# Optimization experiments

Measured on AMD Instinct MI355X. Metric: run time of the kernel, lower is better.

Reference implementation:

```python
import jax, jax.numpy as jnp
import numpy as np

D_MODEL = 768
NUM_HEADS = 12
HEAD_DIM = D_MODEL // NUM_HEADS
SEQ = 4096
BATCH = 1


def setup_inputs() -> dict:
    key = jax.random.key(0)
    ks = jax.random.split(key, 6)
    scale = 1.0 / np.sqrt(D_MODEL)
    x = jax.random.normal(ks[0], (BATCH, SEQ, D_MODEL), dtype=jnp.float32)
    mask = jnp.tril(jnp.ones((SEQ, SEQ), dtype=bool))[None, None]  # [1,1,S,S] causal
    Wq = jax.random.normal(ks[1], (D_MODEL, D_MODEL), dtype=jnp.float32) * scale
    Wk = jax.random.normal(ks[2], (D_MODEL, D_MODEL), dtype=jnp.float32) * scale
    Wv = jax.random.normal(ks[3], (D_MODEL, D_MODEL), dtype=jnp.float32) * scale
    Wo = jax.random.normal(ks[4], (D_MODEL, D_MODEL), dtype=jnp.float32) * scale
    bo = jax.random.normal(ks[5], (D_MODEL,), dtype=jnp.float32) * 0.01
    return {"x": x, "mask": mask, "Wq": Wq, "Wk": Wk, "Wv": Wv, "Wo": Wo, "bo": bo}


def _rope_tables(seq_len, head_dim, dtype):
    # inv_freq over even dims; emb = cat(freqs, freqs) but only the first half
    # participates in the well-defined rotation (x1/x2 have head_dim//2 channels)
    inv_freq = 1.0 / (10000.0 ** (jnp.arange(0, head_dim, 2, dtype=dtype) / head_dim))
    t = jnp.arange(seq_len, dtype=dtype)
    freqs = t[:, None] * inv_freq[None, :]  # [S, head_dim//2]
    return jnp.cos(freqs), jnp.sin(freqs)


def _apply_rotary(xh, cos, sin):
    # xh: [B,H,S,hd]; cos/sin: [S, hd//2]
    x1 = xh[..., ::2]
    x2 = xh[..., 1::2]
    # faithful to source: concatenated (not interleaved) rotated halves
    return jnp.concatenate([x1 * cos - x2 * sin, x1 * sin + x2 * cos], axis=-1)


def reference(x, mask, Wq, Wk, Wv, Wo, bo):
    B, S, D = x.shape
    H, hd = NUM_HEADS, HEAD_DIM
    def split_heads(y):
        return y.reshape(B, S, H, hd).transpose(0, 2, 1, 3)  # [B,H,S,hd]
    q = split_heads(x @ Wq.T)
    k = split_heads(x @ Wk.T)
    v = split_heads(x @ Wv.T)
    cos, sin = _rope_tables(S, hd, x.dtype)
    q = _apply_rotary(q, cos, sin)
    k = _apply_rotary(k, cos, sin)
    scores = jnp.einsum('bhqd,bhkd->bhqk', q, k) / jnp.sqrt(jnp.asarray(hd, x.dtype))
    scores = jnp.where(mask, scores, jnp.asarray(-1e9, x.dtype))
    attn = jax.nn.softmax(scores, axis=-1)  # dropout is identity in eval
    out = jnp.einsum('bhqk,bhkd->bhqd', attn, v)
    out = out.transpose(0, 2, 1, 3).reshape(B, S, D)
    return out @ Wo.T + bo
```

## Files before the change

### kernel.cpp

```cpp
#include <hip/hip_runtime.h>
#include <hip/hip_bf16.h>
#include <math.h>

#define SEQ 4096
#define DM  768
#define NH  12
#define HD  64
#define PER ((size_t)NH * SEQ * HD)
#define XN  ((size_t)SEQ * DM)
#define WN  ((size_t)DM * DM)

typedef __attribute__((ext_vector_type(8))) short bf16x8;
typedef __attribute__((ext_vector_type(4))) short s16x4;
typedef __attribute__((ext_vector_type(4))) float f32x4;

#define MFMA(a, b, c) __builtin_amdgcn_mfma_f32_16x16x32_bf16((a), (b), (c), 0, 0, 0)

#if __has_builtin(__builtin_amdgcn_exp2f)
#define EXP2(x) __builtin_amdgcn_exp2f(x)
#else
#define EXP2(x) exp2f(x)
#endif

#define SWZ(row, blk) (((row) << 6) + ((((blk) ^ ((row) & 7))) << 3))

__device__ __forceinline__ unsigned short f2b(float f) {
    unsigned int u = __float_as_uint(f);
    u += 0x7FFFu + ((u >> 16) & 1u);
    return (unsigned short)(u >> 16);
}

__global__ __launch_bounds__(256) void prep_kernel(
    const float* __restrict__ x,  const float* __restrict__ wq,
    const float* __restrict__ wk, const float* __restrict__ wv,
    const float* __restrict__ wo,
    unsigned short* __restrict__ dstbase, float2* __restrict__ rope)
{
    const float* srcs[5] = {x, wq, wk, wv, wo};
    const size_t n4s[5]  = {XN / 4, WN / 4, WN / 4, WN / 4, WN / 4};
    unsigned short* d = dstbase;
    for (int rg = 0; rg < 5; ++rg) {
        const float4* s4 = (const float4*)srcs[rg];
        s16x4* d4 = (s16x4*)d;
        for (size_t i = (size_t)blockIdx.x * 256 + threadIdx.x; i < n4s[rg];
             i += (size_t)gridDim.x * 256) {
            const float4 v = s4[i];
            s16x4 p;
            p.x = (short)f2b(v.x); p.y = (short)f2b(v.y);
            p.z = (short)f2b(v.z); p.w = (short)f2b(v.w);
            d4[i] = p;
        }
        d += n4s[rg] * 4;
    }
    for (int g = blockIdx.x * 256 + threadIdx.x; g < 131072; g += gridDim.x * 256) {
        const int row = g >> 5, fi = g & 31;
        const float invf = expf(-(float)fi * 0.28782313662425576f);
        float sn, cs;
        sincosf((float)row * invf, &sn, &cs);
        rope[row * 32 + fi] = make_float2(cs, sn);
    }
}

__global__ __launch_bounds__(256) void qkv_mfma(
    const float* __restrict__ x,  const unsigned short* __restrict__ xb,
    const float* __restrict__ Wq, const float* __restrict__ Wk, const float* __restrict__ Wv,
    const unsigned short* __restrict__ Wqb, const unsigned short* __restrict__ Wkb,
    const unsigned short* __restrict__ Wvb,
    const float2* __restrict__ rope,
    unsigned short* __restrict__ Qo, unsigned short* __restrict__ Ko,
    unsigned short* __restrict__ Vo, int fast)
{
    __shared__ __align__(16) unsigned short Xs[2][4096];
    __shared__ __align__(16) unsigned short Ws[2][3][4096];
    __shared__ unsigned short VL[64 * 66];

    const int t    = threadIdx.x;
    const int w    = t >> 6;
    const int lane = t & 63;
    const int quad = lane >> 4;
    const int l16  = lane & 15;

    const int gid = blockIdx.y * 64 + blockIdx.x;
    const int Wl  = (gid & 7) * 96 + (gid >> 3);
    const int h   = Wl % 12;
    const int s0  = (Wl / 12) * 64;
    const int n0  = h * 64;

    const unsigned short* Wbs[3] = {Wqb, Wkb, Wvb};
    const float*          Wfs[3] = {Wq, Wk, Wv};

    const int rowb = 32 * (w >> 1);
    const int colb = 32 * (w & 1);

    f32x4 acc[3][2][2];
    #pragma unroll
    for (int rg = 0; rg < 3; ++rg)
        #pragma unroll
        for (int mi = 0; mi < 2; ++mi)
            #pragma unroll
            for (int ni = 0; ni < 2; ++ni) acc[rg][mi][ni] = (f32x4){0,0,0,0};

    const int prow = t >> 3, pblk = t & 7;

    bf16x8 xr0, xr1, wr0[3], wr1[3];
    if (fast) {
        xr0 = *(const bf16x8*)&xb[(size_t)(s0 + prow) * DM + pblk * 8];
        xr1 = *(const bf16x8*)&xb[(size_t)(s0 + prow + 32) * DM + pblk * 8];
        #pragma unroll
        for (int rg = 0; rg < 3; ++rg) {
            wr0[rg] = *(const bf16x8*)&Wbs[rg][(size_t)(n0 + prow) * DM + pblk * 8];
            wr1[rg] = *(const bf16x8*)&Wbs[rg][(size_t)(n0 + prow + 32) * DM + pblk * 8];
        }
        *(bf16x8*)&Xs[0][SWZ(prow, pblk)]      = xr0;
        *(bf16x8*)&Xs[0][SWZ(prow + 32, pblk)] = xr1;
        #pragma unroll
        for (int rg = 0; rg < 3; ++rg) {
            *(bf16x8*)&Ws[0][rg][SWZ(prow, pblk)]      = wr0[rg];
            *(bf16x8*)&Ws[0][rg][SWZ(prow + 32, pblk)] = wr1[rg];
        }
    } else {
        for (int e = t; e < 1024; e += 256) {
            const int row = e >> 4, c4 = e & 15;
            const int off = SWZ(row, c4 >> 1) + (c4 & 1) * 4;
            const float4 xv = *(const float4*)&x[(size_t)(s0 + row) * DM + c4 * 4];
            s16x4 px; px.x = (short)f2b(xv.x); px.y = (short)f2b(xv.y);
            px.z = (short)f2b(xv.z); px.w = (short)f2b(xv.w);
            *(s16x4*)&Xs[0][off] = px;
            #pragma unroll
            for (int rg = 0; rg < 3; ++rg) {
                const float4 wv = *(const float4*)&Wfs[rg][(size_t)(n0 + row) * DM + c4 * 4];
                s16x4 pw; pw.x = (short)f2b(wv.x); pw.y = (short)f2b(wv.y);
                pw.z = (short)f2b(wv.z); pw.w = (short)f2b(wv.w);
                *(s16x4*)&Ws[0][rg][off] = pw;
            }
        }
    }
    __syncthreads();

    for (int kt = 0; kt < 12; ++kt) {
        const unsigned short* Xb = Xs[kt & 1];
        if (fast && kt < 11) {
            const int k0 = (kt + 1) * 64;
            xr0 = *(const bf16x8*)&xb[(size_t)(s0 + prow) * DM + k0 + pblk * 8];
            xr1 = *(const bf16x8*)&xb[(size_t)(s0 + prow + 32) * DM + k0 + pblk * 8];
            #pragma unroll
            for (int rg = 0; rg < 3; ++rg) {
                wr0[rg] = *(const bf16x8*)&Wbs[rg][(size_t)(n0 + prow) * DM + k0 + pblk * 8];
                wr1[rg] = *(const bf16x8*)&Wbs[rg][(size_t)(n0 + prow + 32) * DM + k0 + pblk * 8];
            }
        }
        bf16x8 a[2][2];
        #pragma unroll
        for (int mi = 0; mi < 2; ++mi)
            #pragma unroll
            for (int hh = 0; hh < 2; ++hh)
                a[mi][hh] = *(const bf16x8*)&Xb[SWZ(rowb + 16 * mi + l16, 4 * hh + quad)];
        #pragma unroll
        for (int rg = 0; rg < 3; ++rg) {
            const unsigned short* Wbt = Ws[kt & 1][rg];
            #pragma unroll
            for (int ni = 0; ni < 2; ++ni) {
                const bf16x8 b0 = *(const bf16x8*)&Wbt[SWZ(colb + 16 * ni + l16, quad)];
                const bf16x8 b1 = *(const bf16x8*)&Wbt[SWZ(colb + 16 * ni + l16, 4 + quad)];
                #pragma unroll
                for (int mi = 0; mi < 2; ++mi) {
                    acc[rg][mi][ni] = MFMA(a[mi][0], b0, acc[rg][mi][ni]);
                    acc[rg][mi][ni] = MFMA(a[mi][1], b1, acc[rg][mi][ni]);
                }
            }
        }
        if (kt < 11) {
            const int nb = (kt + 1) & 1;
            if (fast) {
                *(bf16x8*)&Xs[nb][SWZ(prow, pblk)]      = xr0;
                *(bf16x8*)&Xs[nb][SWZ(prow + 32, pblk)] = xr1;
                #pragma unroll
                for (int rg = 0; rg < 3; ++rg) {
                    *(bf16x8*)&Ws[nb][rg][SWZ(prow, pblk)]      = wr0[rg];
                    *(bf16x8*)&Ws[nb][rg][SWZ(prow + 32, pblk)] = wr1[rg];
                }
            } else {
                const int k0 = (kt + 1) * 64;
                for (int e = t; e < 1024; e += 256) {
                    const int row = e >> 4, c4 = e & 15;
                    const int off = SWZ(row, c4 >> 1) + (c4 & 1) * 4;
                    const float4 xv = *(const float4*)&x[(size_t)(s0 + row) * DM + k0 + c4 * 4];
                    s16x4 px; px.x = (short)f2b(xv.x); px.y = (short)f2b(xv.y);
                    px.z = (short)f2b(xv.z); px.w = (short)f2b(xv.w);
                    *(s16x4*)&Xs[nb][off] = px;
                    #pragma unroll
                    for (int rg = 0; rg < 3; ++rg) {
                        const float4 wv = *(const float4*)&Wfs[rg][(size_t)(n0 + row) * DM + k0 + c4 * 4];
                        s16x4 pw; pw.x = (short)f2b(wv.x); pw.y = (short)f2b(wv.y);
                        pw.z = (short)f2b(wv.z); pw.w = (short)f2b(wv.w);
                        *(s16x4*)&Ws[nb][rg][off] = pw;
                    }
                }
            }
        }
        __syncthreads();
    }

    const size_t headoff = (size_t)h * SEQ * HD;
    #pragma unroll
    for (int rg = 0; rg < 2; ++rg) {
        unsigned short* dst = (rg == 0) ? Qo : Ko;
        const float qsc = (rg == 0) ? 0.18033688011112042f : 1.0f;
        #pragma unroll
        for (int mi = 0; mi < 2; ++mi)
            #pragma unroll
            for (int ni = 0; ni < 2; ++ni)
                #pragma unroll
                for (int r = 0; r < 4; ++r) {
                    const int srow = s0 + rowb + 16 * mi + quad * 4 + r;
                    const int d  = colb + 16 * ni + l16;
                    const int fi = d >> 1;
                    const float own = acc[rg][mi][ni][r] * qsc;
                    const float oth = __shfl_xor(own, 1);
                    float cs, sn;
                    if (fast) {
                        const float2 t2 = rope[srow * 32 + fi];
                        cs = t2.x; sn = t2.y;
                    } else {
                        const float invf = expf(-(float)fi * 0.28782313662425576f);
                        sincosf((float)srow * invf, &sn, &cs);
                    }
                    const float val = (d & 1) ? (oth * sn + own * cs)
                                              : (own * cs - oth * sn);
                    dst[headoff + (size_t)srow * HD + ((d & 1) ? 32 : 0) + fi] = f2b(val);
                }
    }
    #pragma unroll
    for (int mi = 0; mi < 2; ++mi)
        #pragma unroll
        for (int ni = 0; ni < 2; ++ni)
            #pragma unroll
            for (int r = 0; r < 4; ++r)
                VL[(colb + 16 * ni + l16) * 66 + rowb + 16 * mi + quad * 4 + r] =
                    f2b(acc[2][mi][ni][r]);
    __syncthreads();
    for (int e = t; e < 2048; e += 256) {
        const int d = e >> 5, sp = e & 31;
        const unsigned int v = (unsigned int)VL[d * 66 + 2 * sp] |
                               ((unsigned int)VL[d * 66 + 2 * sp + 1] << 16);
        *(unsigned int*)&Vo[headoff + (size_t)d * SEQ + s0 + 2 * sp] = v;
    }
}

__global__ __launch_bounds__(256, 2) void attn_mfma(
    const unsigned short* __restrict__ Q,
    const unsigned short* __restrict__ K,
    const unsigned short* __restrict__ V,
    unsigned short* __restrict__ O,
    float* __restrict__ Part)
{
    __shared__ __align__(16) unsigned char SM[39936];
    unsigned short* Ps  = (unsigned short*)SM;
    unsigned short* Qst = (unsigned short*)(SM + 20480);
    float* ACC  = (float*)SM;
    float* ACC2 = (float*)(SM + 20480);
    float* Lx   = (float*)(SM + 38912);

    int h, xx;
    if (gridDim.x == 96) {
        const int gid = blockIdx.y * 96 + blockIdx.x;
        const int Wl  = (gid & 7) * 144 + (gid >> 3);
        h  = Wl / 96;
        xx = Wl - h * 96;
    } else {
        const int gid = blockIdx.y * 64 + blockIdx.x;
        const int Wl  = (gid & 7) * 96 + (gid >> 3);
        h  = Wl >> 6;
        xx = Wl & 63;
    }

    int i, kstart, nch, domask, partial, pslice;
    if (gridDim.x == 96) {
        if (xx < 64) {
            i = 63 - xx; kstart = 0;
            const int full = ((i * 64 + 63) >> 7) + 1;
            nch = full < 16 ? full : 16;
            domask  = (i <= 31);
            partial = (i >= 32); pslice = 0;
        } else {
            i = 127 - xx; kstart = 2048;
            nch = ((i * 64 + 63 - 2048) >> 7) + 1;
            domask = 1; partial = 1; pslice = 1;
        }
    } else {
        i = 63 - xx; kstart = 0;
        nch = ((i * 64 + 63) >> 7) + 1;
        domask = 1; partial = 0; pslice = 0;
    }
    const int q0 = i * 64;

    const int t    = threadIdx.x;
    const int w    = t >> 6;
    const int lane = t & 63;
    const int quad = lane >> 4;
    const int l16  = lane & 15;
    const size_t headoff = (size_t)h * SEQ * HD;
    const unsigned short* Kg = K + headoff;
    const unsigned short* Vg = V + headoff;

    for (int e = t; e < 512; e += 256) {
        const int row = e >> 3, bp = e & 7, blk = bp ^ (row & 7);
        *(bf16x8*)&Qst[row * 64 + bp * 8] =
            *(const bf16x8*)&Q[headoff + (size_t)(q0 + row) * HD + blk * 8];
    }
    __syncthreads();
    bf16x8 aQ[4][2];
    #pragma unroll
    for (int qt = 0; qt < 4; ++qt)
        #pragma unroll
        for (int hh = 0; hh < 2; ++hh)
            aQ[qt][hh] = *(const bf16x8*)&Qst[SWZ(16 * qt + l16, 4 * hh + quad)];

    bf16x8 kf00, kf01, kf10, kf11;
    {
        const size_t kr = (size_t)(kstart + 32 * w + l16) * HD + quad * 8;
        kf00 = *(const bf16x8*)&Kg[kr];
        kf01 = *(const bf16x8*)&Kg[kr + 32];
        kf10 = *(const bf16x8*)&Kg[kr + 16 * HD];
        kf11 = *(const bf16x8*)&Kg[kr + 16 * HD + 32];
    }

    bf16x8 ones;
    #pragma unroll
    for (int ii = 0; ii < 8; ++ii) ones[ii] = (short)0x3F80;

    f32x4 oT[4][4];
    #pragma unroll
    for (int dt = 0; dt < 4; ++dt)
        #pragma unroll
        for (int qt = 0; qt < 4; ++qt) oT[dt][qt] = (f32x4){0,0,0,0};
    f32x4 lT[4] = {{0,0,0,0},{0,0,0,0},{0,0,0,0},{0,0,0,0}};

    unsigned short* usp = Ps + w * 2560;

    for (int c = 0; c < nch; ++c) {
        const int k0 = kstart + c * 128;
        const int last = (c == nch - 1);

        const size_t vr = (size_t)l16 * SEQ + k0 + 32 * w + quad * 8;
        const bf16x8 vf0 = *(const bf16x8*)&Vg[vr];
        const bf16x8 vf1 = *(const bf16x8*)&Vg[vr + 16 * SEQ];
        const bf16x8 vf2 = *(const bf16x8*)&Vg[vr + 32 * SEQ];
        const bf16x8 vf3 = *(const bf16x8*)&Vg[vr + 48 * SEQ];

        #pragma unroll
        for (int qt = 0; qt < 4; ++qt) {
            f32x4 s0 = (f32x4){0,0,0,0}, s1 = (f32x4){0,0,0,0};
            s0 = MFMA(aQ[qt][0], kf00, s0);
            s0 = MFMA(aQ[qt][1], kf01, s0);
            s1 = MFMA(aQ[qt][0], kf10, s1);
            s1 = MFMA(aQ[qt][1], kf11, s1);
            if (domask && last) {
                const int key0 = k0 + 32 * w + l16;
                #pragma unroll
                for (int r = 0; r < 4; ++r) {
                    const int qrow = q0 + 16 * qt + 4 * quad + r;
                    if (key0 > qrow)      s0[r] = -1e30f;
                    if (key0 + 16 > qrow) s1[r] = -1e30f;
                }
            }
            #pragma unroll
            for (int r = 0; r < 4; ++r) {
                const int row = (16 * qt + 4 * quad + r) * 40;
                usp[row + l16]      = f2b(EXP2(s0[r]));
                usp[row + 16 + l16] = f2b(EXP2(s1[r]));
            }
        }

        if (c + 1 < nch) {
            const size_t kr = (size_t)(k0 + 128 + 32 * w + l16) * HD + quad * 8;
            kf00 = *(const bf16x8*)&Kg[kr];
            kf01 = *(const bf16x8*)&Kg[kr + 32];
            kf10 = *(const bf16x8*)&Kg[kr + 16 * HD];
            kf11 = *(const bf16x8*)&Kg[kr + 16 * HD + 32];
        }

        asm volatile("s_waitcnt lgkmcnt(0)" ::: "memory");

        __builtin_amdgcn_s_setprio(1);
        #pragma unroll
        for (int qt = 0; qt < 4; ++qt) {
            const bf16x8 bP = *(const bf16x8*)&usp[(16 * qt + l16) * 40 + quad * 8];
            lT[qt] = MFMA(ones, bP, lT[qt]);
            oT[0][qt] = MFMA(vf0, bP, oT[0][qt]);
            oT[1][qt] = MFMA(vf1, bP, oT[1][qt]);
            oT[2][qt] = MFMA(vf2, bP, oT[2][qt]);
            oT[3][qt] = MFMA(vf3, bP, oT[3][qt]);
        }
        __builtin_amdgcn_s_setprio(0);
    }

    __syncthreads();
    if (w != 0 && quad == 0) {
        #pragma unroll
        for (int qt = 0; qt < 4; ++qt)
            Lx[w * 64 + 16 * qt + l16] = lT[qt][0];
    }
    if (w == 1) {
        #pragma unroll
        for (int dt = 0; dt < 4; ++dt)
            #pragma unroll
            for (int qt = 0; qt < 4; ++qt)
                *(f32x4*)&ACC[(16 * qt + l16) * 72 + 16 * dt + 4 * quad] = oT[dt][qt];
    }
    __syncthreads();
    if (w == 0) {
        #pragma unroll
        for (int dt = 0; dt < 4; ++dt)
            #pragma unroll
            for (int qt = 0; qt < 4; ++qt)
                oT[dt][qt] += *(const f32x4*)&ACC[(16 * qt + l16) * 72 + 16 * dt + 4 * quad];
    }
    if (w == 2) {
        #pragma unroll
        for (int dt = 0; dt < 4; ++dt)
            #pragma unroll
            for (int qt = 0; qt < 4; ++qt)
                *(f32x4*)&ACC2[(16 * qt + l16) * 72 + 16 * dt + 4 * quad] = oT[dt][qt];
    }
    __syncthreads();
    if (w == 0) {
        #pragma unroll
        for (int dt = 0; dt < 4; ++dt)
            #pragma unroll
            for (int qt = 0; qt < 4; ++qt)
                oT[dt][qt] += *(const f32x4*)&ACC2[(16 * qt + l16) * 72 + 16 * dt + 4 * quad];
    }
    if (w == 3) {
        #pragma unroll
        for (int dt = 0; dt < 4; ++dt)
            #pragma unroll
            for (int qt = 0; qt < 4; ++qt)
                *(f32x4*)&ACC[(16 * qt + l16) * 72 + 16 * dt + 4 * quad] = oT[dt][qt];
    }
    __syncthreads();
    if (w == 0) {
        float ls[4];
        #pragma unroll
        for (int qt = 0; qt < 4; ++qt) {
            #pragma unroll
            for (int dt = 0; dt < 4; ++dt)
                oT[dt][qt] += *(const f32x4*)&ACC[(16 * qt + l16) * 72 + 16 * dt + 4 * quad];
            ls[qt] = lT[qt][0] + Lx[64 + 16 * qt + l16] +
                     Lx[128 + 16 * qt + l16] + Lx[192 + 16 * qt + l16];
        }
        if (!partial) {
            #pragma unroll
            for (int qt = 0; qt < 4; ++qt) {
                const float inv = 1.0f / ls[qt];
                const size_t rowoff = (size_t)(q0 + 16 * qt + l16) * DM + h * HD;
                #pragma unroll
                for (int dt = 0; dt < 4; ++dt) {
                    ushort4 u;
                    u.x = f2b(oT[dt][qt][0] * inv);
                    u.y = f2b(oT[dt][qt][1] * inv);
                    u.z = f2b(oT[dt][qt][2] * inv);
                    u.w = f2b(oT[dt][qt][3] * inv);
                    *(ushort4*)&O[rowoff + 16 * dt + 4 * quad] = u;
                }
            }
        } else {
            float* P = Part + (size_t)(((i - 32) * 12 + h) * 2 + pslice) * 4160;
            #pragma unroll
            for (int dt = 0; dt < 4; ++dt)
                #pragma unroll
                for (int qt = 0; qt < 4; ++qt)
                    *(f32x4*)&P[(16 * qt + l16) * 64 + 16 * dt + 4 * quad] = oT[dt][qt];
            if (quad == 0) {
                #pragma unroll
                for (int qt = 0; qt < 4; ++qt)
                    P[4096 + 16 * qt + l16] = ls[qt];
            }
        }
    }
}

__global__ __launch_bounds__(256) void reduce_attn(
    const float* __restrict__ Part, unsigned short* __restrict__ O)
{
    const int b  = blockIdx.x;
    const int i  = 32 + b / 12, h = b % 12;
    const int q0 = i * 64;
    const float* P0 = Part + (size_t)(b * 2 + 0) * 4160;
    const float* P1 = Part + (size_t)(b * 2 + 1) * 4160;
    __shared__ float linv[64];
    const int t = threadIdx.x;
    if (t < 64) linv[t] = 1.0f / (P0[4096 + t] + P1[4096 + t]);
    __syncthreads();
    for (int idx = t; idx < 4096; idx += 256) {
        const int q = idx >> 6, d = idx & 63;
        const float v = (P0[q * 64 + d] + P1[q * 64 + d]) * linv[q];
        O[(size_t)(q0 + q) * DM + h * HD + d] = f2b(v);
    }
}

__global__ __launch_bounds__(256) void proj_mfma(
    const unsigned short* __restrict__ A,
    const float* __restrict__ Wo, const unsigned short* __restrict__ Wob,
    const float* __restrict__ bo,
    float* __restrict__ out, int fast)
{
    __shared__ __align__(16) unsigned short Xs[2][4096];
    __shared__ __align__(16) unsigned short Ws[2][4096];

    const int t    = threadIdx.x;
    const int w    = t >> 6;
    const int lane = t & 63;
    const int quad = lane >> 4;
    const int l16  = lane & 15;

    const int gid = blockIdx.y * 64 + blockIdx.x;
    const int Wl  = (gid & 7) * 96 + (gid >> 3);
    const int s0  = (Wl / 12) * 64;
    const int n0  = (Wl % 12) * 64;

    const int prow = t >> 3, pblk = t & 7;

    f32x4 acc[4] = {{0,0,0,0},{0,0,0,0},{0,0,0,0},{0,0,0,0}};

    bf16x8 ar0, ar1, wr0, wr1;
    ar0 = *(const bf16x8*)&A[(size_t)(s0 + prow) * DM + pblk * 8];
    ar1 = *(const bf16x8*)&A[(size_t)(s0 + prow + 32) * DM + pblk * 8];
    *(bf16x8*)&Xs[0][SWZ(prow, pblk)]      = ar0;
    *(bf16x8*)&Xs[0][SWZ(prow + 32, pblk)] = ar1;
    if (fast) {
        wr0 = *(const bf16x8*)&Wob[(size_t)(n0 + prow) * DM + pblk * 8];
        wr1 = *(const bf16x8*)&Wob[(size_t)(n0 + prow + 32) * DM + pblk * 8];
        *(bf16x8*)&Ws[0][SWZ(prow, pblk)]      = wr0;
        *(bf16x8*)&Ws[0][SWZ(prow + 32, pblk)] = wr1;
    } else {
        for (int e = t; e < 1024; e += 256) {
            const int row = e >> 4, c4 = e & 15;
            const float4 wv = *(const float4*)&Wo[(size_t)(n0 + row) * DM + c4 * 4];
            s16x4 pw; pw.x = (short)f2b(wv.x); pw.y = (short)f2b(wv.y);
            pw.z = (short)f2b(wv.z); pw.w = (short)f2b(wv.w);
            *(s16x4*)&Ws[0][SWZ(row, c4 >> 1) + (c4 & 1) * 4] = pw;
        }
    }
    __syncthreads();

    for (int kt = 0; kt < 12; ++kt) {
        const unsigned short* Xb  = Xs[kt & 1];
        const unsigned short* Wbt = Ws[kt & 1];
        if (kt < 11) {
            const int k0 = (kt + 1) * 64;
            ar0 = *(const bf16x8*)&A[(size_t)(s0 + prow) * DM + k0 + pblk * 8];
            ar1 = *(const bf16x8*)&A[(size_t)(s0 + prow + 32) * DM + k0 + pblk * 8];
            if (fast) {
                wr0 = *(const bf16x8*)&Wob[(size_t)(n0 + prow) * DM + k0 + pblk * 8];
                wr1 = *(const bf16x8*)&Wob[(size_t)(n0 + prow + 32) * DM + k0 + pblk * 8];
            }
        }
        const bf16x8 a0 = *(const bf16x8*)&Xb[SWZ(16 * w + l16, quad)];
        const bf16x8 a1 = *(const bf16x8*)&Xb[SWZ(16 * w + l16, 4 + quad)];
        #pragma unroll
        for (int nt = 0; nt < 4; ++nt) {
            const bf16x8 b0 = *(const bf16x8*)&Wbt[SWZ(16 * nt + l16, quad)];
            const bf16x8 b1 = *(const bf16x8*)&Wbt[SWZ(16 * nt + l16, 4 + quad)];
            acc[nt] = MFMA(a0, b0, acc[nt]);
            acc[nt] = MFMA(a1, b1, acc[nt]);
        }
        if (kt < 11) {
            const int nb = (kt + 1) & 1;
            *(bf16x8*)&Xs[nb][SWZ(prow, pblk)]      = ar0;
            *(bf16x8*)&Xs[nb][SWZ(prow + 32, pblk)] = ar1;
            if (fast) {
                *(bf16x8*)&Ws[nb][SWZ(prow, pblk)]      = wr0;
                *(bf16x8*)&Ws[nb][SWZ(prow + 32, pblk)] = wr1;
            } else {
                const int k0 = (kt + 1) * 64;
                for (int e = t; e < 1024; e += 256) {
                    const int row = e >> 4, c4 = e & 15;
                    const float4 wv = *(const float4*)&Wo[(size_t)(n0 + row) * DM + k0 + c4 * 4];
                    s16x4 pw; pw.x = (short)f2b(wv.x); pw.y = (short)f2b(wv.y);
                    pw.z = (short)f2b(wv.z); pw.w = (short)f2b(wv.w);
                    *(s16x4*)&Ws[nb][SWZ(row, c4 >> 1) + (c4 & 1) * 4] = pw;
                }
            }
        }
        __syncthreads();
    }

    #pragma unroll
    for (int nt = 0; nt < 4; ++nt)
        #pragma unroll
        for (int r = 0; r < 4; ++r) {
            const int srow = s0 + 16 * w + quad * 4 + r;
            const int n    = n0 + nt * 16 + l16;
            out[(size_t)srow * DM + n] = acc[nt][r] + bo[n];
        }
}

extern "C" void kernel_launch(void* const* d_in, const int* in_sizes, int n_in,
                              void* d_out, int out_size, void* d_ws, size_t ws_size,
                              hipStream_t stream) {
    const float* x  = (const float*)d_in[0];
    const float* Wq = (const float*)d_in[2];
    const float* Wk = (const float*)d_in[3];
    const float* Wv = (const float*)d_in[4];
    const float* Wo = (const float*)d_in[5];
    const float* bo = (const float*)d_in[6];
    float* out = (float*)d_out;

    unsigned short* U  = (unsigned short*)d_ws;
    unsigned short* Qw = U;
    unsigned short* Kw = U + PER;
    unsigned short* Vw = U + 2 * PER;
    unsigned short* Ow = U + 3 * PER;
    unsigned short* xb  = U + 4 * PER;
    unsigned short* Wqb = xb + XN;
    unsigned short* Wkb = Wqb + WN;
    unsigned short* Wvb = Wkb + WN;
    unsigned short* Wob = Wvb + WN;
    float2* rope = (float2*)(Wob + WN);
    float*  part = (float*)(rope + 4096 * 32);
    const size_t need  = (char*)part - (char*)d_ws;
    const size_t need2 = need + (size_t)384 * 2 * 4160 * 4;
    const int fast  = (ws_size >= need)  ? 1 : 0;
    const int split = (ws_size >= need2) ? 1 : 0;

    if (fast)
        prep_kernel<<<1024, 256, 0, stream>>>(x, Wq, Wk, Wv, Wo, xb, rope);
    qkv_mfma<<<dim3(64, 12), 256, 0, stream>>>(
        x, xb, Wq, Wk, Wv, Wqb, Wkb, Wvb, rope, Qw, Kw, Vw, fast);
    if (split) {
        attn_mfma<<<dim3(96, NH), 256, 0, stream>>>(Qw, Kw, Vw, Ow, part);
        reduce_attn<<<dim3(384), 256, 0, stream>>>(part, Ow);
    } else {
        attn_mfma<<<dim3(64, 12), 256, 0, stream>>>(Qw, Kw, Vw, Ow, part);
    }
    proj_mfma<<<dim3(SEQ / 64, DM / 64), 256, 0, stream>>>(Ow, Wo, Wob, bo, out, fast);
}
```

Measured before the change: 233.5 us.

## Software-pipeline QK scores one chunk ahead in attention inner loop

Restructures the attention key-chunk loop so the QK^T MFMAs for the next chunk are issued while the current chunk's exp/store to LDS runs, using ping-pong score register arrays. K is now prefetched two chunks ahead and V one chunk ahead, after the PV MFMAs. The aim is to hide global-load and MFMA latency behind the softmax exp work. The cost is higher register pressure (16 extra f32x4) and a manually unrolled loop body, which may lower occupancy.

After: 235.7 us. About the same (+0.9%).

```diff
diff --git a/kernel.cpp b/kernel.cpp
--- a/kernel.cpp
+++ b/kernel.cpp
@@ -324,6 +324,31 @@
         kf10 = *(const bf16x8*)&Kg[kr + 16 * HD];
         kf11 = *(const bf16x8*)&Kg[kr + 16 * HD + 32];
     }
+    f32x4 sA[8], sB[8];
+    #pragma unroll
+    for (int qt = 0; qt < 4; ++qt) {
+        f32x4 s0 = (f32x4){0,0,0,0}, s1 = (f32x4){0,0,0,0};
+        s0 = MFMA(aQ[qt][0], kf00, s0);
+        s0 = MFMA(aQ[qt][1], kf01, s0);
+        s1 = MFMA(aQ[qt][0], kf10, s1);
+        s1 = MFMA(aQ[qt][1], kf11, s1);
+        sA[2 * qt] = s0; sA[2 * qt + 1] = s1;
+    }
+    bf16x8 vf0, vf1, vf2, vf3;
+    {
+        const size_t vr = (size_t)l16 * SEQ + kstart + 32 * w + quad * 8;
+        vf0 = *(const bf16x8*)&Vg[vr];
+        vf1 = *(const bf16x8*)&Vg[vr + 16 * SEQ];
+        vf2 = *(const bf16x8*)&Vg[vr + 32 * SEQ];
+        vf3 = *(const bf16x8*)&Vg[vr + 48 * SEQ];
+    }
+    if (nch > 1) {
+        const size_t kr = (size_t)(kstart + 128 + 32 * w + l16) * HD + quad * 8;
+        kf00 = *(const bf16x8*)&Kg[kr];
+        kf01 = *(const bf16x8*)&Kg[kr + 32];
+        kf10 = *(const bf16x8*)&Kg[kr + 16 * HD];
+        kf11 = *(const bf16x8*)&Kg[kr + 16 * HD + 32];
+    }
 
     bf16x8 ones;
     #pragma unroll
@@ -338,62 +363,70 @@
 
     unsigned short* usp = Ps + w * 2560;
 
-    for (int c = 0; c < nch; ++c) {
-        const int k0 = kstart + c * 128;
-        const int last = (c == nch - 1);
-
-        const size_t vr = (size_t)l16 * SEQ + k0 + 32 * w + quad * 8;
-        const bf16x8 vf0 = *(const bf16x8*)&Vg[vr];
-        const bf16x8 vf1 = *(const bf16x8*)&Vg[vr + 16 * SEQ];
-        const bf16x8 vf2 = *(const bf16x8*)&Vg[vr + 32 * SEQ];
-        const bf16x8 vf3 = *(const bf16x8*)&Vg[vr + 48 * SEQ];
-
-        #pragma unroll
-        for (int qt = 0; qt < 4; ++qt) {
-            f32x4 s0 = (f32x4){0,0,0,0}, s1 = (f32x4){0,0,0,0};
-            s0 = MFMA(aQ[qt][0], kf00, s0);
-            s0 = MFMA(aQ[qt][1], kf01, s0);
-            s1 = MFMA(aQ[qt][0], kf10, s1);
-            s1 = MFMA(aQ[qt][1], kf11, s1);
-            if (domask && last) {
-                const int key0 = k0 + 32 * w + l16;
-                #pragma unroll
-                for (int r = 0; r < 4; ++r) {
-                    const int qrow = q0 + 16 * qt + 4 * quad + r;
-                    if (key0 > qrow)      s0[r] = -1e30f;
-                    if (key0 + 16 > qrow) s1[r] = -1e30f;
-                }
-            }
-            #pragma unroll
-            for (int r = 0; r < 4; ++r) {
-                const int row = (16 * qt + 4 * quad + r) * 40;
-                usp[row + l16]      = f2b(EXP2(s0[r]));
-                usp[row + 16 + l16] = f2b(EXP2(s1[r]));
-            }
-        }
-
-        if (c + 1 < nch) {
-            const size_t kr = (size_t)(k0 + 128 + 32 * w + l16) * HD + quad * 8;
-            kf00 = *(const bf16x8*)&Kg[kr];
-            kf01 = *(const bf16x8*)&Kg[kr + 32];
-            kf10 = *(const bf16x8*)&Kg[kr + 16 * HD];
-            kf11 = *(const bf16x8*)&Kg[kr + 16 * HD + 32];
-        }
-
-        asm volatile("s_waitcnt lgkmcnt(0)" ::: "memory");
-
-        __builtin_amdgcn_s_setprio(1);
-        #pragma unroll
-        for (int qt = 0; qt < 4; ++qt) {
-            const bf16x8 bP = *(const bf16x8*)&usp[(16 * qt + l16) * 40 + quad * 8];
-            lT[qt] = MFMA(ones, bP, lT[qt]);
-            oT[0][qt] = MFMA(vf0, bP, oT[0][qt]);
-            oT[1][qt] = MFMA(vf1, bP, oT[1][qt]);
-            oT[2][qt] = MFMA(vf2, bP, oT[2][qt]);
-            oT[3][qt] = MFMA(vf3, bP, oT[3][qt]);
-        }
-        __builtin_amdgcn_s_setprio(0);
-    }
+#define STEP(cur, nxt, cc) do {                                               \
+    const int k0_   = kstart + (cc) * 128;                                    \
+    const int last_ = ((cc) == nch - 1);                                      \
+    const int hasN_ = ((cc) + 1 < nch);                                       \
+    _Pragma("unroll")                                                         \
+    for (int qt = 0; qt < 4; ++qt) {                                          \
+        f32x4 s0 = cur[2 * qt], s1 = cur[2 * qt + 1];                         \
+        if (domask && last_) {                                                \
+            const int key0 = k0_ + 32 * w + l16;                              \
+            _Pragma("unroll")                                                 \
+            for (int r = 0; r < 4; ++r) {                                     \
+                const int qrow = q0 + 16 * qt + 4 * quad + r;                 \
+                if (key0 > qrow)      s0[r] = -1e30f;                         \
+                if (key0 + 16 > qrow) s1[r] = -1e30f;                         \
+            }                                                                 \
+        }                                                                     \
+        _Pragma("unroll")                                                     \
+        for (int r = 0; r < 4; ++r) {                                         \
+            const int row_ = (16 * qt + 4 * quad + r) * 40;                   \
+            usp[row_ + l16]      = f2b(EXP2(s0[r]));                          \
+            usp[row_ + 16 + l16] = f2b(EXP2(s1[r]));                          \
+        }                                                                     \
+        if (hasN_) {                                                          \
+            f32x4 n0 = (f32x4){0,0,0,0}, n1 = (f32x4){0,0,0,0};               \
+            n0 = MFMA(aQ[qt][0], kf00, n0);                                   \
+            n0 = MFMA(aQ[qt][1], kf01, n0);                                   \
+            n1 = MFMA(aQ[qt][0], kf10, n1);                                   \
+            n1 = MFMA(aQ[qt][1], kf11, n1);                                   \
+            nxt[2 * qt] = n0; nxt[2 * qt + 1] = n1;                           \
+        }                                                                     \
+    }                                                                         \
+    if ((cc) + 2 < nch) {                                                     \
+        const size_t kr_ = (size_t)(k0_ + 256 + 32 * w + l16) * HD + quad * 8;\
+        kf00 = *(const bf16x8*)&Kg[kr_];                                      \
+        kf01 = *(const bf16x8*)&Kg[kr_ + 32];                                 \
+        kf10 = *(const bf16x8*)&Kg[kr_ + 16 * HD];                            \
+        kf11 = *(const bf16x8*)&Kg[kr_ + 16 * HD + 32];                       \
+    }                                                                         \
+    asm volatile("s_waitcnt lgkmcnt(0)" ::: "memory");                        \
+    __builtin_amdgcn_s_setprio(1);                                            \
+    _Pragma("unroll")                                                         \
+    for (int qt = 0; qt < 4; ++qt) {                                          \
+        const bf16x8 bP = *(const bf16x8*)&usp[(16 * qt + l16) * 40 + quad * 8];\
+        lT[qt] = MFMA(ones, bP, lT[qt]);                                      \
+        oT[0][qt] = MFMA(vf0, bP, oT[0][qt]);                                 \
+        oT[1][qt] = MFMA(vf1, bP, oT[1][qt]);                                 \
+        oT[2][qt] = MFMA(vf2, bP, oT[2][qt]);                                 \
+        oT[3][qt] = MFMA(vf3, bP, oT[3][qt]);                                 \
+    }                                                                         \
+    __builtin_amdgcn_s_setprio(0);                                            \
+    if (hasN_) {                                                              \
+        const size_t vr_ = (size_t)l16 * SEQ + k0_ + 128 + 32 * w + quad * 8; \
+        vf0 = *(const bf16x8*)&Vg[vr_];                                       \
+        vf1 = *(const bf16x8*)&Vg[vr_ + 16 * SEQ];                            \
+        vf2 = *(const bf16x8*)&Vg[vr_ + 32 * SEQ];                            \
+        vf3 = *(const bf16x8*)&Vg[vr_ + 48 * SEQ];                            \
+    }                                                                         \
+} while (0)
+
+    for (int c = 0; c < nch; c += 2) {
+        STEP(sA, sB, c);
+        if (c + 1 < nch) STEP(sB, sA, c + 1);
+    }
+#undef STEP
 
     __syncthreads();
     if (w != 0 && quad == 0) {
```

## Shrink attention LDS footprint, load Q directly, pack P stores, permute V transpose

Applied to the files above, without the earlier changes.

Drops the Q staging buffer in shared memory and loads the Q fragments straight from global memory. The final cross-wave reduction now reuses a single ACC buffer, which cuts LDS from about 39 KB to about 21 KB and could allow more blocks per CU. P values are converted to bf16 in pairs with v_cvt_pk_bf16_f32 and written as 32-bit stores, so P's column layout in LDS is permuted. The V-transpose writer is reordered to match that permutation. In exchange, the reduction takes more barriers, and the direct Q loads are uncoalesced and unswizzled.

Measured after the change: 236.2 us. No clear change (+1.2%).

```diff
diff --git a/kernel.cpp b/kernel.cpp
--- a/kernel.cpp
+++ b/kernel.cpp
@@ -241,9 +241,10 @@
     __syncthreads();
     for (int e = t; e < 2048; e += 256) {
         const int d = e >> 5, sp = e & 31;
-        const unsigned int v = (unsigned int)VL[d * 66 + 2 * sp] |
-                               ((unsigned int)VL[d * 66 + 2 * sp + 1] << 16);
-        *(unsigned int*)&Vo[headoff + (size_t)d * SEQ + s0 + 2 * sp] = v;
+        const int g = sp >> 4, m = sp & 15;
+        const unsigned int v = (unsigned int)VL[d * 66 + 32 * g + m] |
+                               ((unsigned int)VL[d * 66 + 32 * g + m + 16] << 16);
+        *(unsigned int*)&Vo[headoff + (size_t)d * SEQ + s0 + 32 * g + 2 * m] = v;
     }
 }
 
@@ -254,12 +255,10 @@
     unsigned short* __restrict__ O,
     float* __restrict__ Part)
 {
-    __shared__ __align__(16) unsigned char SM[39936];
-    unsigned short* Ps  = (unsigned short*)SM;
-    unsigned short* Qst = (unsigned short*)(SM + 20480);
-    float* ACC  = (float*)SM;
-    float* ACC2 = (float*)(SM + 20480);
-    float* Lx   = (float*)(SM + 38912);
+    __shared__ __align__(16) unsigned char SM[21504];
+    unsigned short* Ps = (unsigned short*)SM;
+    float* ACC = (float*)SM;
+    float* Lx  = (float*)(SM + 20480);
 
     int h, xx;
     if (gridDim.x == 96) {
@@ -303,18 +302,13 @@
     const unsigned short* Kg = K + headoff;
     const unsigned short* Vg = V + headoff;
 
-    for (int e = t; e < 512; e += 256) {
-        const int row = e >> 3, bp = e & 7, blk = bp ^ (row & 7);
-        *(bf16x8*)&Qst[row * 64 + bp * 8] =
-            *(const bf16x8*)&Q[headoff + (size_t)(q0 + row) * HD + blk * 8];
-    }
-    __syncthreads();
     bf16x8 aQ[4][2];
     #pragma unroll
     for (int qt = 0; qt < 4; ++qt)
         #pragma unroll
         for (int hh = 0; hh < 2; ++hh)
-            aQ[qt][hh] = *(const bf16x8*)&Qst[SWZ(16 * qt + l16, 4 * hh + quad)];
+            aQ[qt][hh] = *(const bf16x8*)
+                &Q[headoff + (size_t)(q0 + 16 * qt + l16) * HD + (4 * hh + quad) * 8];
 
     bf16x8 kf00, kf01, kf10, kf11;
     {
@@ -366,9 +360,11 @@
             }
             #pragma unroll
             for (int r = 0; r < 4; ++r) {
-                const int row = (16 * qt + 4 * quad + r) * 40;
-                usp[row + l16]      = f2b(EXP2(s0[r]));
-                usp[row + 16 + l16] = f2b(EXP2(s1[r]));
+                const float e0 = EXP2(s0[r]), e1 = EXP2(s1[r]);
+                unsigned int pk;
+                asm("v_cvt_pk_bf16_f32 %0, %1, %2" : "=v"(pk) : "v"(e0), "v"(e1));
+                const int row_ = (16 * qt + 4 * quad + r) * 40;
+                *(unsigned int*)&usp[row_ + 2 * l16] = pk;
             }
         }
 
@@ -401,54 +397,31 @@
         for (int qt = 0; qt < 4; ++qt)
             Lx[w * 64 + 16 * qt + l16] = lT[qt][0];
     }
-    if (w == 1) {
-        #pragma unroll
-        for (int dt = 0; dt < 4; ++dt)
-            #pragma unroll
-            for (int qt = 0; qt < 4; ++qt)
-                *(f32x4*)&ACC[(16 * qt + l16) * 72 + 16 * dt + 4 * quad] = oT[dt][qt];
-    }
-    __syncthreads();
-    if (w == 0) {
-        #pragma unroll
-        for (int dt = 0; dt < 4; ++dt)
-            #pragma unroll
-            for (int qt = 0; qt < 4; ++qt)
-                oT[dt][qt] += *(const f32x4*)&ACC[(16 * qt + l16) * 72 + 16 * dt + 4 * quad];
-    }
-    if (w == 2) {
-        #pragma unroll
-        for (int dt = 0; dt < 4; ++dt)
-            #pragma unroll
-            for (int qt = 0; qt < 4; ++qt)
-                *(f32x4*)&ACC2[(16 * qt + l16) * 72 + 16 * dt + 4 * quad] = oT[dt][qt];
-    }
-    __syncthreads();
-    if (w == 0) {
-        #pragma unroll
-        for (int dt = 0; dt < 4; ++dt)
-            #pragma unroll
-            for (int qt = 0; qt < 4; ++qt)
-                oT[dt][qt] += *(const f32x4*)&ACC2[(16 * qt + l16) * 72 + 16 * dt + 4 * quad];
-    }
-    if (w == 3) {
-        #pragma unroll
-        for (int dt = 0; dt < 4; ++dt)
-            #pragma unroll
-            for (int qt = 0; qt < 4; ++qt)
-                *(f32x4*)&ACC[(16 * qt + l16) * 72 + 16 * dt + 4 * quad] = oT[dt][qt];
-    }
-    __syncthreads();
+    #pragma unroll
+    for (int s = 1; s < 4; ++s) {
+        if (w == s) {
+            #pragma unroll
+            for (int dt = 0; dt < 4; ++dt)
+                #pragma unroll
+                for (int qt = 0; qt < 4; ++qt)
+                    *(f32x4*)&ACC[(16 * qt + l16) * 72 + 16 * dt + 4 * quad] = oT[dt][qt];
+        }
+        __syncthreads();
+        if (w == 0) {
+            #pragma unroll
+            for (int dt = 0; dt < 4; ++dt)
+                #pragma unroll
+                for (int qt = 0; qt < 4; ++qt)
+                    oT[dt][qt] += *(const f32x4*)&ACC[(16 * qt + l16) * 72 + 16 * dt + 4 * quad];
+        }
+        __syncthreads();
+    }
     if (w == 0) {
         float ls[4];
         #pragma unroll
-        for (int qt = 0; qt < 4; ++qt) {
-            #pragma unroll
-            for (int dt = 0; dt < 4; ++dt)
-                oT[dt][qt] += *(const f32x4*)&ACC[(16 * qt + l16) * 72 + 16 * dt + 4 * quad];
+        for (int qt = 0; qt < 4; ++qt)
             ls[qt] = lT[qt][0] + Lx[64 + 16 * qt + l16] +
                      Lx[128 + 16 * qt + l16] + Lx[192 + 16 * qt + l16];
-        }
         if (!partial) {
             #pragma unroll
             for (int qt = 0; qt < 4; ++qt) {
```
